# Optimization experiments

Hardware: AMD Instinct MI355X
Metric: run time of the kernel (lower is better)

Reference implementation:

```python
import jax, jax.numpy as jnp
import numpy as np

H = 128      # hidden_size
V = 32000    # vocab_size
B = 64       # batch
S = 128      # seq_len
EOS = 2
EPS = 1e-12


def setup_inputs() -> dict:
    key = jax.random.key(0)
    k1, k2, k3, k4 = jax.random.split(key, 4)
    input_ids = jax.random.randint(k1, (B, S), 0, V)
    # replicate SOHMM.__init__ (sep_token_id=None branch)
    alpha_exp = jax.nn.softmax(jax.random.normal(k2, (H, H, H)), axis=2)
    alpha_exp = alpha_exp.at[:, -1, :].set(1e-10).at[:, -1, -1].set(1.0)
    beta = jax.nn.log_softmax(jax.random.normal(k3, (H, V)), axis=1)
    beta = beta.at[-1, EOS].set(1e10).at[:-1, EOS].set(-1e10)
    beta = jax.nn.log_softmax(beta, axis=-1)
    gamma = jax.nn.log_softmax(jax.random.normal(k4, (H, H)).reshape(-1)).reshape(H, H)
    return {"input_ids": input_ids, "alpha_exp": alpha_exp, "beta": beta, "gamma": gamma}


def reference(input_ids, alpha_exp, beta, gamma):
    """Faithful jax port of SOHMM.forward. Returns (ys_stacked [S,H,H,B], y_final [B]).
    ys_stacked[t] corresponds to the list entry appended at time step S-1-t... i.e. ys in
    the same order as the torch list (first entry = t=S-1, last = t=0)."""
    batch, seq_len = input_ids.shape
    gamma_exp = jax.nn.softmax(gamma.reshape(-1)).reshape(gamma.shape)
    ids = input_ids.T  # [S, B]
    # input_probs[t, h, b] = beta[h, ids[t, b]], masked where id == -1
    input_probs = jnp.transpose(beta[:, ids], (1, 0, 2))  # [S, H, B]
    input_probs = jnp.where((ids != -1)[:, None, :], input_probs, 0.0)

    # t = S-1 step: y = 0 + input_probs[S-1] broadcast over leading H
    y0 = jnp.zeros((alpha_exp.shape[0],) + input_probs.shape[1:][::1][-2:][:0], dtype=input_probs.dtype)  # placeholder
    y0 = jnp.broadcast_to(input_probs[seq_len - 1][None], (alpha_exp.shape[0],) + input_probs[seq_len - 1].shape)

    def step(y, ip_t):
        # numerically-stable log-space second-order transition
        y_max = y.max(axis=(0, 1), keepdims=True)          # [1,1,B]
        y_exp = jnp.exp(y - y_max)
        y_new = jnp.einsum('ijk,jkb->ijb', alpha_exp, y_exp)
        y_new = jnp.log(y_new + EPS) + y_max
        y_new = y_new + ip_t[None]
        return y_new, y_new

    ips = input_probs[seq_len - 2::-1]  # t = S-2 down to 0
    y_last, ys_rest = jax.lax.scan(step, y0, ips)
    ys = jnp.concatenate([y0[None], ys_rest], axis=0)  # [S, H, H, B]

    y_max = y_last.max(axis=(0, 1))  # [B]
    y_final = jnp.log(jnp.einsum('ij,ijb->b', gamma_exp, jnp.exp(y_last - y_max[None, None])) + EPS) + y_max
    return ys, y_final
```

## Files before the change

kernel.cpp:

```cpp
#include <hip/hip_runtime.h>


#define Hd 128
#define Bd 64
#define Sd 128
#define Vd 32000
#define HBc (Hd * Bd)
#define HHBc (Hd * Hd * Bd)
#define NBLK 256
#define NTHR 1024
#define EPSF 1e-12f
#define FTAG 200u
#define SLOTW ((size_t)NBLK * Bd)

typedef __attribute__((ext_vector_type(4))) float f32x4;
typedef __attribute__((ext_vector_type(8))) short s16x8;
typedef __attribute__((ext_vector_type(4))) short s16x4;

__device__ __forceinline__ short f2bf(float f) {
  unsigned u = __builtin_bit_cast(unsigned, f);
  unsigned r = (u + 0x7fffu + ((u >> 16) & 1u)) >> 16;
  return (short)(r & 0xffffu);
}

__device__ __forceinline__ unsigned mono_enc(float f) {
  unsigned u = __builtin_bit_cast(unsigned, f);
  return u ^ ((u & 0x80000000u) ? 0xFFFFFFFFu : 0x80000000u);
}
__device__ __forceinline__ float mono_dec(unsigned m) {
  unsigned u = (m & 0x80000000u) ? (m ^ 0x80000000u) : ~m;
  return __builtin_bit_cast(float, u);
}
__device__ __forceinline__ unsigned packM(float f, unsigned tag) {
  return (tag << 24) | (mono_enc(f) >> 8);
}
__device__ __forceinline__ float decM(unsigned w) {
  return mono_dec((w & 0x00FFFFFFu) << 8);
}
__device__ __forceinline__ unsigned pack_y(float v, unsigned tag) {
  unsigned u = __builtin_bit_cast(unsigned, v);
  return ((u + 0x80u) & 0xFFFFFF00u) | tag;
}
__device__ __forceinline__ float as_f(unsigned u) { return __builtin_bit_cast(float, u); }
__device__ __forceinline__ unsigned pack24(float f, unsigned tag) {
  unsigned u = __builtin_bit_cast(unsigned, f);
  return ((u + 0x80u) & 0xFFFFFF00u) | tag;
}
__device__ __forceinline__ float dec24(unsigned v) {
  return __builtin_bit_cast(float, v & 0xFFFFFF00u);
}

__device__ __forceinline__ unsigned ld_u32(const unsigned* p) {
  return __hip_atomic_load(p, __ATOMIC_RELAXED, __HIP_MEMORY_SCOPE_AGENT);
}
__device__ __forceinline__ void st_u32(unsigned* p, unsigned v) {
  __hip_atomic_store(p, v, __ATOMIC_RELAXED, __HIP_MEMORY_SCOPE_AGENT);
}

__global__ __launch_bounds__(NTHR) void sohmm_persistent(
    const int* __restrict__ ids, const float* __restrict__ alpha,
    const float* __restrict__ beta, const float* __restrict__ gamma,
    float* __restrict__ out, unsigned* __restrict__ mslot,
    unsigned* __restrict__ fpart) {
  const int tid = threadIdx.x;
  const int bid = blockIdx.x;
  const int j = bid >> 1;
  const int ih = bid & 1;
  const int lane = tid & 63;
  const int w = tid >> 6;
  const int l15 = lane & 15;
  const int g4 = lane >> 4;
  const int wi = w >> 2;
  const int wb = w & 3;
  const int ti0 = ih * 64 + wi * 16;
  const int tb0 = wb * 16;
  const int sb = tid & 63;
  const int sq = tid >> 6;

  __shared__ __align__(16) short ET[64][132];
  __shared__ __align__(16) float ip_all[Sd][Bd];
  __shared__ unsigned redS[16][64];
  __shared__ float redF[16][64];
  __shared__ float wred[4][64];
  __shared__ float gex[128];
  __shared__ float MbS[64];

  s16x8 afrag[4];
  {
    const int i = ti0 + l15;
    const float* ap = alpha + ((size_t)i * Hd + j) * Hd;
#pragma unroll
    for (int kc = 0; kc < 4; ++kc) {
      const int k = kc * 32 + g4 * 8;
      f32x4 a0 = *(const f32x4*)(ap + k);
      f32x4 a1 = *(const f32x4*)(ap + k + 4);
      s16x8 f;
      f[0] = f2bf(a0[0]); f[1] = f2bf(a0[1]); f[2] = f2bf(a0[2]); f[3] = f2bf(a0[3]);
      f[4] = f2bf(a1[0]); f[5] = f2bf(a1[1]); f[6] = f2bf(a1[2]); f[7] = f2bf(a1[3]);
      afrag[kc] = f;
    }
  }

  for (int idx = tid; idx < Sd * Bd; idx += NTHR) {
    const int t = idx >> 6, b = idx & 63;
    ip_all[t][b] = beta[(size_t)j * Vd + ids[b * Sd + (Sd - 1 - t)]];
  }
  {
    float m = -3.4e38f;
#pragma unroll
    for (int c = 0; c < 4; ++c) {
      f32x4 g = *(const f32x4*)(gamma + (size_t)(c * NTHR + tid) * 4);
      m = fmaxf(fmaxf(fmaxf(m, g[0]), g[1]), fmaxf(g[2], g[3]));
    }
#pragma unroll
    for (int o = 32; o >= 1; o >>= 1) m = fmaxf(m, __shfl_xor(m, o, 64));
    if (lane == 0) redF[0][w] = m;
  }
  __syncthreads();
  {
    const int r = tid >> 4;
    const int b4 = (tid & 15) * 4;
    unsigned* yw = (unsigned*)out + (size_t)((ih * 64 + r) * Hd + j) * Bd + b4;
#pragma unroll
    for (int e = 0; e < 4; ++e) st_u32(yw + e, pack_y(ip_all[0][b4 + e], 1u));
  }
  if (tid < 64)
    st_u32(mslot + (size_t)bid * Bd + tid, packM(ip_all[0][tid], 1u));
  {
    float gm = redF[0][0];
#pragma unroll
    for (int q = 1; q < 16; ++q) gm = fmaxf(gm, redF[0][q]);
    float ss = 0.f;
#pragma unroll
    for (int c = 0; c < 4; ++c) {
      f32x4 g = *(const f32x4*)(gamma + (size_t)(c * NTHR + tid) * 4);
      ss += __expf(g[0] - gm) + __expf(g[1] - gm) + __expf(g[2] - gm) + __expf(g[3] - gm);
    }
#pragma unroll
    for (int o = 32; o >= 1; o >>= 1) ss += __shfl_xor(ss, o, 64);
    if (lane == 0) redF[1][w] = ss;
    __syncthreads();
    float gs = 0.f;
#pragma unroll
    for (int q = 0; q < 16; ++q) gs += redF[1][q];
    if (tid < 128) gex[tid] = __expf(gamma[(size_t)tid * Hd + j] - gm) * (1.f / gs);
  }
  {
    const unsigned tg = 1u;
    const unsigned* pm = mslot + (size_t)(sq * 16) * Bd + sb;
    unsigned g[16];
#pragma unroll
    for (int q = 0; q < 16; ++q) g[q] = ld_u32(pm + (size_t)q * Bd);
    unsigned spins = 0;
    for (;;) {
      unsigned bad = 0;
#pragma unroll
      for (int q = 0; q < 16; ++q) bad |= (g[q] >> 24) ^ tg;
      if (!bad) break;
      if (++spins > (1u << 18)) break;
      __builtin_amdgcn_s_sleep(1);
#pragma unroll
      for (int q = 0; q < 16; ++q)
        if ((g[q] >> 24) != tg) g[q] = ld_u32(pm + (size_t)q * Bd);
    }
    unsigned mx = 0u;
#pragma unroll
    for (int q = 0; q < 16; ++q) mx = g[q] > mx ? g[q] : mx;
    redS[sq][sb] = mx;
  }
  __syncthreads();
  if (tid < 64) {
    unsigned mx = 0u;
#pragma unroll
    for (int q = 0; q < 16; ++q) mx = redS[q][tid] > mx ? redS[q][tid] : mx;
    MbS[tid] = decM(mx);
  }
  __syncthreads();

  float val[4];
#pragma unroll 1
  for (int s = 1; s < Sd; ++s) {
    const unsigned ytag = (unsigned)(2 * s - 1);
    const unsigned wtag = (unsigned)(2 * s + 1);

    const int k0 = sq * 8;
    const unsigned* ypw = (const unsigned*)out + (size_t)(s - 1) * HHBc + (size_t)j * HBc + sb;
    unsigned g[8];
#pragma unroll
    for (int e = 0; e < 8; ++e) g[e] = ld_u32(ypw + (size_t)(k0 + e) * Bd);
    {
      unsigned spins = 0;
      for (;;) {
        unsigned bad = 0;
#pragma unroll
        for (int e = 0; e < 8; ++e) bad |= (g[e] & 0xFFu) ^ ytag;
        if (!bad) break;
        if (++spins > (1u << 18)) break;
        __builtin_amdgcn_s_sleep(1);
#pragma unroll
        for (int e = 0; e < 8; ++e)
          if ((g[e] & 0xFFu) != ytag) g[e] = ld_u32(ypw + (size_t)(k0 + e) * Bd);
      }
    }

    {
      const float Mv = MbS[sb];
      union { s16x8 v; } u;
#pragma unroll
      for (int e = 0; e < 8; ++e)
        ((short*)&u.v)[e] = f2bf(__expf(fminf(as_f(g[e]) - Mv, 1.0f)));
      *(s16x8*)&ET[sb][k0] = u.v;
    }
    __syncthreads();

    f32x4 acc = (f32x4){0.f, 0.f, 0.f, 0.f};
#pragma unroll
    for (int kc = 0; kc < 4; ++kc) {
      const int bb = tb0 + l15;
      const int kk = kc * 32 + g4 * 8;
      union { s16x4 h[2]; s16x8 v; } u;
      u.h[0] = *(const s16x4*)&ET[bb][kk];
      u.h[1] = *(const s16x4*)&ET[bb][kk + 4];
      acc = __builtin_amdgcn_mfma_f32_16x16x32_bf16(afrag[kc], u.v, acc, 0, 0, 0);
    }

    {
      unsigned* ycw = (unsigned*)out + (size_t)s * HHBc;
      const int b = tb0 + l15;
      const float add = MbS[b] + ip_all[s][b];
      float mx = -3.4e38f;
#pragma unroll
      for (int r = 0; r < 4; ++r) {
        float vv = __logf(acc[r] + EPSF) + add;
        val[r] = vv;
        st_u32(ycw + (size_t)(ti0 + g4 * 4 + r) * HBc + j * Bd + b, pack_y(vv, wtag));
        mx = fmaxf(mx, vv);
      }
      mx = fmaxf(mx, __shfl_xor(mx, 16, 64));
      mx = fmaxf(mx, __shfl_xor(mx, 32, 64));
      if (lane < 16) wred[wi][tb0 + lane] = mx;
    }
    __syncthreads();
    if (tid < 64) {
      float m = fmaxf(fmaxf(wred[0][tid], wred[1][tid]), fmaxf(wred[2][tid], wred[3][tid]));
      st_u32(mslot + (size_t)(s & 7) * SLOTW + (size_t)bid * Bd + tid,
             packM(m, (unsigned)s + 1u));
    }

    {
      const unsigned tg = (s >= 2) ? (unsigned)s : 1u;
      const unsigned* pm = mslot + (size_t)((tg - 1u) & 7u) * SLOTW + (size_t)(sq * 16) * Bd + sb;
      unsigned g2[16];
#pragma unroll
      for (int q = 0; q < 16; ++q) g2[q] = ld_u32(pm + (size_t)q * Bd);
      unsigned spins = 0;
      for (;;) {
        unsigned bad = 0;
#pragma unroll
        for (int q = 0; q < 16; ++q) bad |= (g2[q] >> 24) ^ tg;
        if (!bad) break;
        if (++spins > (1u << 18)) break;
        __builtin_amdgcn_s_sleep(1);
#pragma unroll
        for (int q = 0; q < 16; ++q)
          if ((g2[q] >> 24) != tg) g2[q] = ld_u32(pm + (size_t)q * Bd);
      }
      unsigned mx = 0u;
#pragma unroll
      for (int q = 0; q < 16; ++q) mx = g2[q] > mx ? g2[q] : mx;
      redS[sq][sb] = mx;
    }
    __syncthreads();
    if (tid < 64) {
      unsigned mx = 0u;
#pragma unroll
      for (int q = 0; q < 16; ++q) mx = redS[q][tid] > mx ? redS[q][tid] : mx;
      MbS[tid] = decM(mx);
    }
    __syncthreads();
  }

  {
    const int b = tb0 + l15;
    const float M = MbS[b];
    float sum = 0.f;
#pragma unroll
    for (int r = 0; r < 4; ++r)
      sum += gex[ti0 + g4 * 4 + r] * __expf(fminf(val[r] - M, 1.0f));
    sum += __shfl_xor(sum, 16, 64);
    sum += __shfl_xor(sum, 32, 64);
    if (lane < 16) wred[wi][tb0 + lane] = sum;
  }
  __syncthreads();
  if (tid < 64) {
    float sm = wred[0][tid] + wred[1][tid] + wred[2][tid] + wred[3][tid];
    st_u32(fpart + (size_t)bid * Bd + tid, pack24(sm, FTAG));
  }

  if (bid == 0) {
    const unsigned* pm = fpart + (size_t)(sq * 16) * Bd + sb;
    unsigned g[16];
#pragma unroll
    for (int q = 0; q < 16; ++q) g[q] = ld_u32(pm + (size_t)q * Bd);
    {
      unsigned spins = 0;
      for (;;) {
        unsigned bad = 0;
#pragma unroll
        for (int q = 0; q < 16; ++q) bad |= (g[q] & 0xFFu) ^ FTAG;
        if (!bad) break;
        if (++spins > (1u << 18)) break;
        __builtin_amdgcn_s_sleep(1);
#pragma unroll
        for (int q = 0; q < 16; ++q)
          if ((g[q] & 0xFFu) != FTAG) g[q] = ld_u32(pm + (size_t)q * Bd);
      }
    }
    float s16v = 0.f;
#pragma unroll
    for (int q = 0; q < 16; ++q) s16v += dec24(g[q]);
    redF[sq][sb] = s16v;
    __syncthreads();
    if (tid < 64) {
      float tot = 0.f;
#pragma unroll
      for (int q = 0; q < 16; ++q) tot += redF[q][tid];
      out[(size_t)Sd * HHBc + tid] = __logf(tot + EPSF) + MbS[tid];
    }
  }
}

extern "C" void kernel_launch(void* const* d_in, const int* in_sizes, int n_in,
                              void* d_out, int out_size, void* d_ws, size_t ws_size,
                              hipStream_t stream) {
  const int* ids = (const int*)d_in[0];
  const float* alpha = (const float*)d_in[1];
  const float* beta = (const float*)d_in[2];
  const float* gamma = (const float*)d_in[3];
  float* out = (float*)d_out;
  unsigned* mslot = (unsigned*)d_ws;
  unsigned* fpart = mslot + 8 * SLOTW;

  hipMemsetAsync(mslot, 0, (8 * SLOTW + SLOTW) * sizeof(unsigned), stream);
  hipLaunchKernelGGL(sohmm_persistent, dim3(NBLK), dim3(NTHR), 0, stream,
                     ids, alpha, beta, gamma, out, mslot, fpart);
}
```

Measured before the change: 493.4 us.

## Use one block per j with 128 blocks, two MFMA tiles per wave

Halves the persistent grid from 256 to 128 blocks, so each block handles all 128 output rows i for one j instead of splitting them across two blocks. Each wave now computes two 16x16 MFMA tiles covering 32 batch columns, and the per-step max exchange reads 128 instead of 256 mslot entries. The goal is to cut cross-block synchronisation and duplicated ET staging per step, at the cost of more work per block on fewer CUs.

```diff
diff --git a/kernel.cpp b/kernel.cpp
--- a/kernel.cpp
+++ b/kernel.cpp
@@ -7,7 +7,7 @@
 #define Vd 32000
 #define HBc (Hd * Bd)
 #define HHBc (Hd * Hd * Bd)
-#define NBLK 256
+#define NBLK 128
 #define NTHR 1024
 #define EPSF 1e-12f
 #define FTAG 200u
@@ -64,16 +64,16 @@
     unsigned* __restrict__ fpart) {
   const int tid = threadIdx.x;
   const int bid = blockIdx.x;
-  const int j = bid >> 1;
-  const int ih = bid & 1;
+  const int j = bid;
   const int lane = tid & 63;
   const int w = tid >> 6;
   const int l15 = lane & 15;
   const int g4 = lane >> 4;
-  const int wi = w >> 2;
-  const int wb = w & 3;
-  const int ti0 = ih * 64 + wi * 16;
-  const int tb0 = wb * 16;
+  const int it = w & 7;
+  const int bh = w >> 3;
+  const int i0 = it * 16;
+  const int b0 = bh * 32 + l15;
+  const int b1 = b0 + 16;
   const int sb = tid & 63;
   const int sq = tid >> 6;
 
@@ -81,13 +81,13 @@
   __shared__ __align__(16) float ip_all[Sd][Bd];
   __shared__ unsigned redS[16][64];
   __shared__ float redF[16][64];
-  __shared__ float wred[4][64];
+  __shared__ float wred[8][64];
   __shared__ float gex[128];
   __shared__ float MbS[64];
 
   s16x8 afrag[4];
   {
-    const int i = ti0 + l15;
+    const int i = i0 + l15;
     const float* ap = alpha + ((size_t)i * Hd + j) * Hd;
 #pragma unroll
     for (int kc = 0; kc < 4; ++kc) {
@@ -118,11 +118,11 @@
   }
   __syncthreads();
   {
-    const int r = tid >> 4;
-    const int b4 = (tid & 15) * 4;
-    unsigned* yw = (unsigned*)out + (size_t)((ih * 64 + r) * Hd + j) * Bd + b4;
-#pragma unroll
-    for (int e = 0; e < 4; ++e) st_u32(yw + e, pack_y(ip_all[0][b4 + e], 1u));
+    const int r = tid >> 3;
+    const int bb8 = (tid & 7) * 8;
+    unsigned* yw = (unsigned*)out + ((size_t)r * Hd + j) * Bd + bb8;
+#pragma unroll
+    for (int e = 0; e < 8; ++e) st_u32(yw + e, pack_y(ip_all[0][bb8 + e], 1u));
   }
   if (tid < 64)
     st_u32(mslot + (size_t)bid * Bd + tid, packM(ip_all[0][tid], 1u));
@@ -147,25 +147,25 @@
   }
   {
     const unsigned tg = 1u;
-    const unsigned* pm = mslot + (size_t)(sq * 16) * Bd + sb;
-    unsigned g[16];
-#pragma unroll
-    for (int q = 0; q < 16; ++q) g[q] = ld_u32(pm + (size_t)q * Bd);
+    const unsigned* pm = mslot + (size_t)(sq * 8) * Bd + sb;
+    unsigned g[8];
+#pragma unroll
+    for (int q = 0; q < 8; ++q) g[q] = ld_u32(pm + (size_t)q * Bd);
     unsigned spins = 0;
     for (;;) {
       unsigned bad = 0;
 #pragma unroll
-      for (int q = 0; q < 16; ++q) bad |= (g[q] >> 24) ^ tg;
+      for (int q = 0; q < 8; ++q) bad |= (g[q] >> 24) ^ tg;
       if (!bad) break;
       if (++spins > (1u << 18)) break;
       __builtin_amdgcn_s_sleep(1);
 #pragma unroll
-      for (int q = 0; q < 16; ++q)
+      for (int q = 0; q < 8; ++q)
         if ((g[q] >> 24) != tg) g[q] = ld_u32(pm + (size_t)q * Bd);
     }
     unsigned mx = 0u;
 #pragma unroll
-    for (int q = 0; q < 16; ++q) mx = g[q] > mx ? g[q] : mx;
+    for (int q = 0; q < 8; ++q) mx = g[q] > mx ? g[q] : mx;
     redS[sq][sb] = mx;
   }
   __syncthreads();
@@ -177,7 +177,7 @@
   }
   __syncthreads();
 
-  float val[4];
+  float val0[4], val1[4];
 #pragma unroll 1
   for (int s = 1; s < Sd; ++s) {
     const unsigned ytag = (unsigned)(2 * s - 1);
@@ -213,61 +213,74 @@
     }
     __syncthreads();
 
-    f32x4 acc = (f32x4){0.f, 0.f, 0.f, 0.f};
+    f32x4 acc0 = (f32x4){0.f, 0.f, 0.f, 0.f};
+    f32x4 acc1 = (f32x4){0.f, 0.f, 0.f, 0.f};
 #pragma unroll
     for (int kc = 0; kc < 4; ++kc) {
-      const int bb = tb0 + l15;
       const int kk = kc * 32 + g4 * 8;
-      union { s16x4 h[2]; s16x8 v; } u;
-      u.h[0] = *(const s16x4*)&ET[bb][kk];
-      u.h[1] = *(const s16x4*)&ET[bb][kk + 4];
-      acc = __builtin_amdgcn_mfma_f32_16x16x32_bf16(afrag[kc], u.v, acc, 0, 0, 0);
+      union { s16x4 h[2]; s16x8 v; } u0, u1;
+      u0.h[0] = *(const s16x4*)&ET[b0][kk];
+      u0.h[1] = *(const s16x4*)&ET[b0][kk + 4];
+      u1.h[0] = *(const s16x4*)&ET[b1][kk];
+      u1.h[1] = *(const s16x4*)&ET[b1][kk + 4];
+      acc0 = __builtin_amdgcn_mfma_f32_16x16x32_bf16(afrag[kc], u0.v, acc0, 0, 0, 0);
+      acc1 = __builtin_amdgcn_mfma_f32_16x16x32_bf16(afrag[kc], u1.v, acc1, 0, 0, 0);
     }
 
     {
       unsigned* ycw = (unsigned*)out + (size_t)s * HHBc;
-      const int b = tb0 + l15;
-      const float add = MbS[b] + ip_all[s][b];
-      float mx = -3.4e38f;
+      const float add0 = MbS[b0] + ip_all[s][b0];
+      const float add1 = MbS[b1] + ip_all[s][b1];
+      float mx0 = -3.4e38f, mx1 = -3.4e38f;
 #pragma unroll
       for (int r = 0; r < 4; ++r) {
-        float vv = __logf(acc[r] + EPSF) + add;
-        val[r] = vv;
-        st_u32(ycw + (size_t)(ti0 + g4 * 4 + r) * HBc + j * Bd + b, pack_y(vv, wtag));
-        mx = fmaxf(mx, vv);
-      }
-      mx = fmaxf(mx, __shfl_xor(mx, 16, 64));
-      mx = fmaxf(mx, __shfl_xor(mx, 32, 64));
-      if (lane < 16) wred[wi][tb0 + lane] = mx;
+        const size_t row = (size_t)(i0 + g4 * 4 + r) * HBc + (size_t)j * Bd;
+        float v0 = __logf(acc0[r] + EPSF) + add0;
+        float v1 = __logf(acc1[r] + EPSF) + add1;
+        val0[r] = v0; val1[r] = v1;
+        st_u32(ycw + row + b0, pack_y(v0, wtag));
+        st_u32(ycw + row + b1, pack_y(v1, wtag));
+        mx0 = fmaxf(mx0, v0);
+        mx1 = fmaxf(mx1, v1);
+      }
+      mx0 = fmaxf(mx0, __shfl_xor(mx0, 16, 64));
+      mx0 = fmaxf(mx0, __shfl_xor(mx0, 32, 64));
+      mx1 = fmaxf(mx1, __shfl_xor(mx1, 16, 64));
+      mx1 = fmaxf(mx1, __shfl_xor(mx1, 32, 64));
+      if (lane < 16) {
+        wred[it][bh * 32 + lane] = mx0;
+        wred[it][bh * 32 + 16 + lane] = mx1;
+      }
     }
     __syncthreads();
     if (tid < 64) {
-      float m = fmaxf(fmaxf(wred[0][tid], wred[1][tid]), fmaxf(wred[2][tid], wred[3][tid]));
+      float m = wred[0][tid];
+#pragma unroll
+      for (int q = 1; q < 8; ++q) m = fmaxf(m, wred[q][tid]);
       st_u32(mslot + (size_t)(s & 7) * SLOTW + (size_t)bid * Bd + tid,
              packM(m, (unsigned)s + 1u));
     }
-
     {
       const unsigned tg = (s >= 2) ? (unsigned)s : 1u;
-      const unsigned* pm = mslot + (size_t)((tg - 1u) & 7u) * SLOTW + (size_t)(sq * 16) * Bd + sb;
-      unsigned g2[16];
-#pragma unroll
-      for (int q = 0; q < 16; ++q) g2[q] = ld_u32(pm + (size_t)q * Bd);
+      const unsigned* pm = mslot + (size_t)((tg - 1u) & 7u) * SLOTW + (size_t)(sq * 8) * Bd + sb;
+      unsigned g2[8];
+#pragma unroll
+      for (int q = 0; q < 8; ++q) g2[q] = ld_u32(pm + (size_t)q * Bd);
       unsigned spins = 0;
       for (;;) {
         unsigned bad = 0;
 #pragma unroll
-        for (int q = 0; q < 16; ++q) bad |= (g2[q] >> 24) ^ tg;
+        for (int q = 0; q < 8; ++q) bad |= (g2[q] >> 24) ^ tg;
         if (!bad) break;
         if (++spins > (1u << 18)) break;
         __builtin_amdgcn_s_sleep(1);
 #pragma unroll
-        for (int q = 0; q < 16; ++q)
+        for (int q = 0; q < 8; ++q)
           if ((g2[q] >> 24) != tg) g2[q] = ld_u32(pm + (size_t)q * Bd);
       }
       unsigned mx = 0u;
 #pragma unroll
-      for (int q = 0; q < 16; ++q) mx = g2[q] > mx ? g2[q] : mx;
+      for (int q = 0; q < 8; ++q) mx = g2[q] > mx ? g2[q] : mx;
       redS[sq][sb] = mx;
     }
     __syncthreads();
@@ -281,45 +294,53 @@
   }
 
   {
-    const int b = tb0 + l15;
-    const float M = MbS[b];
-    float sum = 0.f;
-#pragma unroll
-    for (int r = 0; r < 4; ++r)
-      sum += gex[ti0 + g4 * 4 + r] * __expf(fminf(val[r] - M, 1.0f));
-    sum += __shfl_xor(sum, 16, 64);
-    sum += __shfl_xor(sum, 32, 64);
-    if (lane < 16) wred[wi][tb0 + lane] = sum;
+    float s0 = 0.f, s1 = 0.f;
+#pragma unroll
+    for (int r = 0; r < 4; ++r) {
+      const float gx = gex[i0 + g4 * 4 + r];
+      s0 += gx * __expf(fminf(val0[r] - MbS[b0], 1.0f));
+      s1 += gx * __expf(fminf(val1[r] - MbS[b1], 1.0f));
+    }
+    s0 += __shfl_xor(s0, 16, 64);
+    s0 += __shfl_xor(s0, 32, 64);
+    s1 += __shfl_xor(s1, 16, 64);
+    s1 += __shfl_xor(s1, 32, 64);
+    if (lane < 16) {
+      wred[it][bh * 32 + lane] = s0;
+      wred[it][bh * 32 + 16 + lane] = s1;
+    }
   }
   __syncthreads();
   if (tid < 64) {
-    float sm = wred[0][tid] + wred[1][tid] + wred[2][tid] + wred[3][tid];
+    float sm = wred[0][tid];
+#pragma unroll
+    for (int q = 1; q < 8; ++q) sm += wred[q][tid];
     st_u32(fpart + (size_t)bid * Bd + tid, pack24(sm, FTAG));
   }
 
   if (bid == 0) {
-    const unsigned* pm = fpart + (size_t)(sq * 16) * Bd + sb;
-    unsigned g[16];
-#pragma unroll
-    for (int q = 0; q < 16; ++q) g[q] = ld_u32(pm + (size_t)q * Bd);
+    const unsigned* pm = fpart + (size_t)(sq * 8) * Bd + sb;
+    unsigned g[8];
+#pragma unroll
+    for (int q = 0; q < 8; ++q) g[q] = ld_u32(pm + (size_t)q * Bd);
     {
       unsigned spins = 0;
       for (;;) {
         unsigned bad = 0;
 #pragma unroll
-        for (int q = 0; q < 16; ++q) bad |= (g[q] & 0xFFu) ^ FTAG;
+        for (int q = 0; q < 8; ++q) bad |= (g[q] & 0xFFu) ^ FTAG;
         if (!bad) break;
         if (++spins > (1u << 18)) break;
         __builtin_amdgcn_s_sleep(1);
 #pragma unroll
-        for (int q = 0; q < 16; ++q)
+        for (int q = 0; q < 8; ++q)
           if ((g[q] & 0xFFu) != FTAG) g[q] = ld_u32(pm + (size_t)q * Bd);
       }
     }
-    float s16v = 0.f;
-#pragma unroll
-    for (int q = 0; q < 16; ++q) s16v += dec24(g[q]);
-    redF[sq][sb] = s16v;
+    float s8 = 0.f;
+#pragma unroll
+    for (int q = 0; q < 8; ++q) s8 += dec24(g[q]);
+    redF[sq][sb] = s8;
     __syncthreads();
     if (tid < 64) {
       float tot = 0.f;
```

Result: slower. 545.1 us (+10.5%).
